# Optimization experiments

Hardware: AMD Instinct MI355X
Metric: run time of the kernel (lower is better)

The kernel has to match this reference:

```python
import jax, jax.numpy as jnp
import numpy as np
from jax import lax

N, T, IN = 64, 1024, 64
H = 512
H2 = H // 2   # 256
H4 = H // 4   # 128
H10 = H // 10 # 51


def _lstm(x, Wih, Whh, bih, bhh):
    """PyTorch-style LSTM, batch_first. x: [N,T,in]. Returns hs [N,T,h], h_T, c_T."""
    n, t, _ = x.shape
    h = Whh.shape[1]
    b = bih + bhh

    def step(carry, xt):
        hprev, cprev = carry
        gates = xt @ Wih.T + hprev @ Whh.T + b
        i, f, g, o = jnp.split(gates, 4, axis=-1)
        i = jax.nn.sigmoid(i)
        f = jax.nn.sigmoid(f)
        g = jnp.tanh(g)
        o = jax.nn.sigmoid(o)
        c = f * cprev + i * g
        hnew = o * jnp.tanh(c)
        return (hnew, c), hnew

    h0 = jnp.zeros((n, h), x.dtype)
    c0 = jnp.zeros((n, h), x.dtype)
    (hT, cT), hs = lax.scan(step, (h0, c0), x.transpose(1, 0, 2))
    return hs.transpose(1, 0, 2), hT, cT


def _causal_self_attention(hs):
    """Unscaled dot-product causal attention, equivalent to the python loop."""
    n, t, h = hs.shape
    scores = jnp.einsum('nth,nsh->nts', hs, hs)  # [N,T,T]
    mask = jnp.tril(jnp.ones((t, t), bool))
    scores = jnp.where(mask[None], scores, -jnp.inf)
    attn = jax.nn.softmax(scores, axis=-1)
    return jnp.einsum('nts,nsh->nth', attn, hs)


def setup_inputs() -> dict:
    key = jax.random.key(0)
    ks = jax.random.split(key, 16)
    s = 0.05
    return {
        'x': jax.random.normal(ks[0], (N, T, IN), jnp.float32),
        'W_ih1': jax.random.normal(ks[1], (4 * H, IN), jnp.float32) * s,
        'W_hh1': jax.random.normal(ks[2], (4 * H, H), jnp.float32) * s,
        'b_ih1': jax.random.normal(ks[3], (4 * H,), jnp.float32) * s,
        'b_hh1': jax.random.normal(ks[4], (4 * H,), jnp.float32) * s,
        'W_ih2': jax.random.normal(ks[5], (4 * H2, H), jnp.float32) * s,
        'W_hh2': jax.random.normal(ks[6], (4 * H2, H2), jnp.float32) * s,
        'b_ih2': jax.random.normal(ks[7], (4 * H2,), jnp.float32) * s,
        'b_hh2': jax.random.normal(ks[8], (4 * H2,), jnp.float32) * s,
        'fc1_w': jax.random.normal(ks[9], (H4, 2 * H2), jnp.float32) * s,
        'fc1_b': jax.random.normal(ks[10], (H4,), jnp.float32) * s,
        'fc2_w': jax.random.normal(ks[11], (H10, H4), jnp.float32) * s,
        'fc2_b': jax.random.normal(ks[12], (H10,), jnp.float32) * s,
        'fc3_w': jax.random.normal(ks[13], (1, H10), jnp.float32) * s,
        'fc3_b': jax.random.normal(ks[14], (1,), jnp.float32) * s,
    }


def reference(x, W_ih1, W_hh1, b_ih1, b_hh1, W_ih2, W_hh2, b_ih2, b_hh2,
              fc1_w, fc1_b, fc2_w, fc2_b, fc3_w, fc3_b):
    out, h1, c1 = _lstm(x, W_ih1, W_hh1, b_ih1, b_hh1)     # [N,T,H]
    out, h2, c2 = _lstm(out, W_ih2, W_hh2, b_ih2, b_hh2)   # [N,T,H2]
    contexts = _causal_self_attention(out)                  # [N,T,H2]
    out = jnp.concatenate((contexts, out), axis=2)          # [N,T,2*H2]
    out = jax.nn.relu(out @ fc1_w.T + fc1_b)                # dropout_ratio=0 -> identity
    out = jax.nn.relu(out @ fc2_w.T + fc2_b)
    out = out @ fc3_w.T + fc3_b                              # [N,T,1]
    return out, h1, c1, h2, c2
```

## Files before the change

### kernel.cpp

```cpp
#include <hip/hip_runtime.h>
#include <hip/hip_bf16.h>

#define N_   64
#define T_   1024
#define IN_  64
#define H1_  512
#define H2_  256
#define NG   4
#define NU1  16
#define NU2  8
#define RING 8
#define RING2 4
#define SENT 0xAAAAAAAAu

typedef __bf16 bf16x8 __attribute__((ext_vector_type(8)));
typedef float  f32x4  __attribute__((ext_vector_type(4)));
typedef unsigned int u32x4 __attribute__((ext_vector_type(4)));
typedef unsigned short u16x8 __attribute__((ext_vector_type(8)));
typedef unsigned long long u64;
typedef __hip_bfloat16 bf16_t;

#define OFF_FLG2  8192u
#define OFF_QUE   12288u
#define ZERO_BYTES 16384u
#define OFF_H1R   16384u
#define OFF_H2R   540672u
#define OFF_XB    671744u
#define OFF_W1    9060352u
#define OFF_W2    11419648u
#define OFF_B1    12992512u
#define OFF_B2    13000704u
#define OFF_FC1W  13004800u
#define OFF_FC2W  13135872u
#define OFF_HS2   13152256u
#define OFF_BURN  46706688u

__device__ __forceinline__ bf16x8 ld16(const bf16_t* p) {
  u32x4 u = *reinterpret_cast<const u32x4*>(p);
  return __builtin_bit_cast(bf16x8, u);
}
__device__ __forceinline__ u64 ld64_mall(const void* p) {
  return __hip_atomic_load((const u64*)p, __ATOMIC_RELAXED, __HIP_MEMORY_SCOPE_AGENT);
}
__device__ __forceinline__ void st4_mall(bf16_t* p, unsigned v) {
  __hip_atomic_store((unsigned*)p, v, __ATOMIC_RELAXED, __HIP_MEMORY_SCOPE_AGENT);
}
__device__ __forceinline__ unsigned ldflag(unsigned* p) {
  return __hip_atomic_load(p, __ATOMIC_RELAXED, __HIP_MEMORY_SCOPE_AGENT);
}
__device__ __forceinline__ bool sentok(u64 w) {
  return ((unsigned)w != SENT) && ((unsigned)(w >> 32) != SENT);
}
__device__ __forceinline__ f32x4 mfma_bf16(bf16x8 a, bf16x8 b, f32x4 c) {
  return __builtin_amdgcn_mfma_f32_16x16x32_bf16(a, b, c, 0, 0, 0);
}
__device__ __forceinline__ float sigf(float x) { return 1.f / (1.f + __expf(-x)); }
__device__ __forceinline__ float tanh_fast(float x) {
  float e = __expf(-2.f * fabsf(x));
  float r = (1.f - e) / (1.f + e);
  return x < 0.f ? -r : r;
}
__device__ __forceinline__ unsigned short bf16_bits(float v) {
  __hip_bfloat16 b = __float2bfloat16(v);
  return *reinterpret_cast<unsigned short*>(&b);
}

__global__ void setup_kernel(const float* __restrict__ x,
    const float* __restrict__ Wih1, const float* __restrict__ Whh1,
    const float* __restrict__ bih1, const float* __restrict__ bhh1,
    const float* __restrict__ Wih2, const float* __restrict__ Whh2,
    const float* __restrict__ bih2, const float* __restrict__ bhh2,
    const float* __restrict__ fc1w, const float* __restrict__ fc2w,
    char* __restrict__ ws)
{
  bf16_t* xb = (bf16_t*)(ws + OFF_XB);
  bf16_t* w1 = (bf16_t*)(ws + OFF_W1);
  bf16_t* w2 = (bf16_t*)(ws + OFF_W2);
  float*  b1 = (float*)(ws + OFF_B1);
  float*  b2 = (float*)(ws + OFF_B2);
  bf16_t* f1 = (bf16_t*)(ws + OFF_FC1W);
  bf16_t* f2 = (bf16_t*)(ws + OFF_FC2W);
  const long E0 = 4194304, E1 = E0 + 1179648, E2 = E1 + 786432,
             E3 = E2 + 2048, E4 = E3 + 1024, E5 = E4 + 65536, E6 = E5 + 8192;
  for (long i = blockIdx.x * (long)blockDim.x + threadIdx.x; i < E6;
       i += (long)gridDim.x * blockDim.x) {
    if (i < E0) {
      xb[i] = __float2bfloat16(x[i]);
    } else if (i < E1) {
      long idx = i - E0; long j = idx / 576, k = idx % 576;
      float v = (k < 64) ? Wih1[j * 64 + k] : Whh1[j * 512 + (k - 64)];
      w1[idx] = __float2bfloat16(v);
    } else if (i < E2) {
      long idx = i - E1; long j = idx / 768, k = idx % 768;
      float v = (k < 512) ? Wih2[j * 512 + k] : Whh2[j * 256 + (k - 512)];
      w2[idx] = __float2bfloat16(v);
    } else if (i < E3) {
      long idx = i - E2; b1[idx] = bih1[idx] + bhh1[idx];
    } else if (i < E4) {
      long idx = i - E3; b2[idx] = bih2[idx] + bhh2[idx];
    } else if (i < E5) {
      long idx = i - E4; f1[idx] = __float2bfloat16(fc1w[idx]);
    } else {
      long idx = i - E5; long j = idx / 128, k = idx % 128;
      f2[idx] = __float2bfloat16(j < 51 ? fc2w[j * 128 + k] : 0.f);
    }
  }
}

__global__ __launch_bounds__(256, 1) void fused_kernel(char* __restrict__ ws,
    const float* __restrict__ fc1b, const float* __restrict__ fc2b,
    const float* __restrict__ fc3w, const float* __restrict__ fc3b,
    float* __restrict__ dout)
{
  const bf16_t* xb  = (const bf16_t*)(ws + OFF_XB);
  const bf16_t* W1  = (const bf16_t*)(ws + OFF_W1);
  const bf16_t* W2  = (const bf16_t*)(ws + OFF_W2);
  const float*  b1  = (const float*)(ws + OFF_B1);
  const float*  b2  = (const float*)(ws + OFF_B2);
  bf16_t* h1r = (bf16_t*)(ws + OFF_H1R);
  bf16_t* h2r = (bf16_t*)(ws + OFF_H2R);
  bf16_t* hs2 = (bf16_t*)(ws + OFF_HS2);
  unsigned* flag2 = (unsigned*)(ws + OFF_FLG2);

  __shared__ __align__(16) char smem[55296];

  const int tid  = threadIdx.x;
  const int wave = tid >> 6;
  const int lane = tid & 63;
  const int l15  = lane & 15;
  const int quad = lane >> 4;
  const int bx   = blockIdx.x;
  const f32x4 z = {0.f, 0.f, 0.f, 0.f};

  if (bx < NG * NU1) {
    const int g = bx >> 4, u = bx & 15, u0 = u * 32;
    bf16_t* hstage = (bf16_t*)smem;
    float*  gbuf   = (float*)(smem + 18688);
    bf16x8 wf[18][2];
    #pragma unroll
    for (int i = 0; i < 18; ++i)
      #pragma unroll
      for (int nt = 0; nt < 2; ++nt)
        wf[i][nt] = ld16(W1 + (size_t)(wave * H1_ + u0 + nt * 16 + l15) * 576 + i * 32 + quad * 8);

    const int sr = tid >> 4;
    const int myp = tid & 15;
    const int row = tid >> 4, ui = (tid & 15) * 2;
    const int nrow = g * 16 + row;
    unsigned* bp = flag2 + (g * NU2 + (tid & 7)) * 32;
    float bi[2], bff[2], bg[2], bo[2], creg[2];
    #pragma unroll
    for (int j = 0; j < 2; ++j) {
      int ug = u0 + ui + j;
      bi[j]  = b1[ug];         bff[j] = b1[H1_ + ug];
      bg[j]  = b1[2*H1_ + ug]; bo[j]  = b1[3*H1_ + ug];
      creg[j] = 0.f;
    }
    #pragma unroll
    for (int s = 0; s < RING; ++s)
      st4_mall(h1r + ((size_t)(g * RING + s) * 16 + row) * 512 + u0 + ui, SENT);

    #pragma unroll 1
    for (int t = 0; t < T_; ++t) {
      {
        u64 xv = *(const u64*)(xb + ((size_t)(g*16 + sr) * T_ + t) * IN_ + myp * 4);
        *(u64*)(hstage + sr * 584 + myp * 4) = xv;
      }
      if (t >= 7)
        while ((int)ldflag(bp) < t - 6) __builtin_amdgcn_s_sleep(1);
      if (t == 0) {
        #pragma unroll
        for (int k = 0; k < 8; ++k)
          *(u64*)(hstage + sr * 584 + 64 + myp * 32 + k * 4) = 0ull;
      } else {
        const u64* src = (const u64*)(h1r + ((size_t)(g * RING + ((t-1) & 7)) * 16 + sr) * 512 + myp * 32);
        u64 w[8];
        for (;;) {
          #pragma unroll
          for (int k = 0; k < 8; ++k) w[k] = ld64_mall(src + k);
          bool ok = true;
          #pragma unroll
          for (int k = 0; k < 8; ++k) ok &= sentok(w[k]);
          if (ok) break;
        }
        #pragma unroll
        for (int k = 0; k < 8; ++k)
          *(u64*)(hstage + sr * 584 + 64 + myp * 32 + k * 4) = w[k];
      }
      __syncthreads();
      st4_mall(h1r + ((size_t)(g * RING + ((t+1) & 7)) * 16 + row) * 512 + u0 + ui, SENT);
      f32x4 acc[2] = {z, z}, acd[2] = {z, z};
      #pragma unroll
      for (int ki = 0; ki < 9; ++ki) {
        bf16x8 aw = ld16(hstage + l15 * 584 + ki * 32 + quad * 8);
        acc[0] = mfma_bf16(aw, wf[ki][0], acc[0]);
        acc[1] = mfma_bf16(aw, wf[ki][1], acc[1]);
      }
      #pragma unroll
      for (int ki = 9; ki < 18; ++ki) {
        bf16x8 aw = ld16(hstage + l15 * 584 + ki * 32 + quad * 8);
        acd[0] = mfma_bf16(aw, wf[ki][0], acd[0]);
        acd[1] = mfma_bf16(aw, wf[ki][1], acd[1]);
      }
      acc[0] += acd[0]; acc[1] += acd[1];
      #pragma unroll
      for (int nt = 0; nt < 2; ++nt)
        #pragma unroll
        for (int r = 0; r < 4; ++r)
          gbuf[(wave * 16 + quad * 4 + r) * 33 + nt * 16 + l15] = acc[nt][r];
      __syncthreads();
      {
        unsigned pack = 0;
        float hv[2];
        #pragma unroll
        for (int j = 0; j < 2; ++j) {
          int col = ui + j;
          float iv = sigf(gbuf[(0*16 + row) * 33 + col] + bi[j]);
          float fv = sigf(gbuf[(1*16 + row) * 33 + col] + bff[j]);
          float gv = tanh_fast(gbuf[(2*16 + row) * 33 + col] + bg[j]);
          float ov = sigf(gbuf[(3*16 + row) * 33 + col] + bo[j]);
          float c = fv * creg[j] + iv * gv;
          creg[j] = c;
          float h = ov * tanh_fast(c);
          hv[j] = h;
          pack |= (unsigned)bf16_bits(h) << (16 * j);
        }
        st4_mall(h1r + ((size_t)(g * RING + (t & 7)) * 16 + row) * 512 + u0 + ui, pack);
        if (t == T_ - 1) {
          #pragma unroll
          for (int j = 0; j < 2; ++j) {
            dout[65536 + nrow * H1_ + u0 + ui + j] = hv[j];
            dout[98304 + nrow * H1_ + u0 + ui + j] = creg[j];
          }
        }
      }
    }
  } else if (bx < NG * NU1 + NG * NU2) {
    const int b2x = bx - NG * NU1;
    const int g = b2x >> 3, u = b2x & 7, u0 = u * 32;
    bf16_t* hstage = (bf16_t*)smem;
    float*  gbuf   = (float*)(smem + 25088);
    bf16x8 wf[24][2];
    #pragma unroll
    for (int i = 0; i < 24; ++i)
      #pragma unroll
      for (int nt = 0; nt < 2; ++nt)
        wf[i][nt] = ld16(W2 + (size_t)(wave * H2_ + u0 + nt * 16 + l15) * 768 + i * 32 + quad * 8);

    const int sr = tid >> 4;
    const int q  = tid & 15;
    const int row = tid >> 4, ui = (tid & 15) * 2;
    const int nrow = g * 16 + row;
    unsigned* myflag = flag2 + (g * NU2 + u) * 32;
    float bi[2], bff[2], bg[2], bo[2], creg[2];
    #pragma unroll
    for (int j = 0; j < 2; ++j) {
      int ug = u0 + ui + j;
      bi[j]  = b2[ug];         bff[j] = b2[H2_ + ug];
      bg[j]  = b2[2*H2_ + ug]; bo[j]  = b2[3*H2_ + ug];
      creg[j] = 0.f;
    }
    #pragma unroll
    for (int s = 0; s < RING2; ++s)
      st4_mall(h2r + ((size_t)(g * RING2 + s) * 16 + row) * 256 + u0 + ui, SENT);

    u64 pf[8];
    #pragma unroll 1
    for (int t = 0; t < T_; ++t) {
      {
        const u64* s1 = (const u64*)(h1r + ((size_t)(g * RING + (t & 7)) * 16 + sr) * 512 + q * 32);
        bool good = (t > 0);
        if (good) {
          #pragma unroll
          for (int k = 0; k < 8; ++k) good &= sentok(pf[k]);
        }
        if (!good) {
          for (;;) {
            #pragma unroll
            for (int k = 0; k < 8; ++k) pf[k] = ld64_mall(s1 + k);
            bool ok = true;
            #pragma unroll
            for (int k = 0; k < 8; ++k) ok &= sentok(pf[k]);
            if (ok) break;
          }
        }
        #pragma unroll
        for (int k = 0; k < 8; ++k)
          *(u64*)(hstage + sr * 784 + q * 32 + k * 4) = pf[k];
      }
      if (t == 0) {
        #pragma unroll
        for (int k = 0; k < 4; ++k)
          *(u64*)(hstage + sr * 784 + 512 + q * 16 + k * 4) = 0ull;
      } else {
        const u64* s2 = (const u64*)(h2r + ((size_t)(g * RING2 + ((t-1) & 3)) * 16 + sr) * 256 + q * 16);
        u64 w[4];
        for (;;) {
          #pragma unroll
          for (int k = 0; k < 4; ++k) w[k] = ld64_mall(s2 + k);
          bool ok = true;
          #pragma unroll
          for (int k = 0; k < 4; ++k) ok &= sentok(w[k]);
          if (ok) break;
        }
        #pragma unroll
        for (int k = 0; k < 4; ++k)
          *(u64*)(hstage + sr * 784 + 512 + q * 16 + k * 4) = w[k];
      }
      __syncthreads();
      if (tid == 0 && t > 0)
        __hip_atomic_store(myflag, (unsigned)t, __ATOMIC_RELAXED, __HIP_MEMORY_SCOPE_AGENT);
      st4_mall(h2r + ((size_t)(g * RING2 + ((t+1) & 3)) * 16 + row) * 256 + u0 + ui, SENT);
      f32x4 acc[2] = {z, z}, acd[2] = {z, z};
      #pragma unroll
      for (int ki = 0; ki < 12; ++ki) {
        bf16x8 aw = ld16(hstage + l15 * 784 + ki * 32 + quad * 8);
        acc[0] = mfma_bf16(aw, wf[ki][0], acc[0]);
        acc[1] = mfma_bf16(aw, wf[ki][1], acc[1]);
      }
      #pragma unroll
      for (int ki = 12; ki < 24; ++ki) {
        bf16x8 aw = ld16(hstage + l15 * 784 + ki * 32 + quad * 8);
        acd[0] = mfma_bf16(aw, wf[ki][0], acd[0]);
        acd[1] = mfma_bf16(aw, wf[ki][1], acd[1]);
      }
      acc[0] += acd[0]; acc[1] += acd[1];
      #pragma unroll
      for (int nt = 0; nt < 2; ++nt)
        #pragma unroll
        for (int r = 0; r < 4; ++r)
          gbuf[(wave * 16 + quad * 4 + r) * 33 + nt * 16 + l15] = acc[nt][r];
      __syncthreads();
      {
        unsigned pack = 0;
        float hv[2];
        #pragma unroll
        for (int j = 0; j < 2; ++j) {
          int col = ui + j;
          float iv = sigf(gbuf[(0*16 + row) * 33 + col] + bi[j]);
          float fv = sigf(gbuf[(1*16 + row) * 33 + col] + bff[j]);
          float gv = tanh_fast(gbuf[(2*16 + row) * 33 + col] + bg[j]);
          float ov = sigf(gbuf[(3*16 + row) * 33 + col] + bo[j]);
          float c = fv * creg[j] + iv * gv;
          creg[j] = c;
          float h = ov * tanh_fast(c);
          hv[j] = h;
          pack |= (unsigned)bf16_bits(h) << (16 * j);
        }
        st4_mall(h2r + ((size_t)(g * RING2 + (t & 3)) * 16 + row) * 256 + u0 + ui, pack);
        st4_mall(hs2 + ((size_t)nrow * T_ + t) * H2_ + u0 + ui, pack);
        if (t == T_ - 1) {
          #pragma unroll
          for (int j = 0; j < 2; ++j) {
            dout[131072 + nrow * H2_ + u0 + ui + j] = hv[j];
            dout[147456 + nrow * H2_ + u0 + ui + j] = creg[j];
          }
        }
      }
      if (t + 1 < T_) {
        const u64* nx = (const u64*)(h1r + ((size_t)(g * RING + ((t+1) & 7)) * 16 + sr) * 512 + q * 32);
        #pragma unroll
        for (int k = 0; k < 8; ++k) pf[k] = ld64_mall(nx + k);
      }
    }
    __syncthreads();
    if (tid == 0)
      __hip_atomic_store(myflag, (unsigned)T_, __ATOMIC_RELAXED, __HIP_MEMORY_SCOPE_AGENT);
  }

  __syncthreads();
  {
    const bf16_t* f1w = (const bf16_t*)(ws + OFF_FC1W);
    const bf16_t* f2w = (const bf16_t*)(ws + OFF_FC2W);
    unsigned* queue = (unsigned*)(ws + OFF_QUE);
    unsigned short* vtile = (unsigned short*)smem;
    bf16_t* plds   = (bf16_t*)(smem + 36864);
    bf16_t* ctxlds = (bf16_t*)smem;
    bf16_t* act1   = (bf16_t*)(smem + 36864);
    float*  act2   = (float*)smem;
    volatile int* itemslot = (volatile int*)(smem + 55040);
    float burn = 1.0f;

    for (;;) {
      if (tid == 0) *itemslot = (int)atomicAdd(queue, 1u);
      __syncthreads();
      const int item = *itemslot;
      __syncthreads();
      if (item >= 1024) break;
      const int qt = item >> 6, n = item & 63, q0 = qt * 64, gg = n >> 4;

      {
        const int need = q0 + 64;
        if (tid < 64) {
          unsigned* p = (lane < NU2) ? flag2 + (gg * NU2 + lane) * 32 : nullptr;
          bool ok = (p == nullptr) || ((int)ldflag(p) >= need);
          while (!__all(ok)) {
            #pragma unroll
            for (int k = 0; k < 32; ++k) burn = fmaf(burn, 1.0000001f, 1e-7f);
            ok = (p == nullptr) || ((int)ldflag(p) >= need);
          }
        }
        __syncthreads();
      }

      bf16x8 aq[8];
      #pragma unroll
      for (int ks = 0; ks < 8; ++ks)
        aq[ks] = ld16(hs2 + ((size_t)n * T_ + q0 + wave * 16 + l15) * H2_ + ks * 32 + quad * 8);
      f32x4 o[16];
      #pragma unroll
      for (int ct = 0; ct < 16; ++ct) o[ct] = z;
      float m_run[4], l_run[4];
      #pragma unroll
      for (int r = 0; r < 4; ++r) { m_run[r] = -1e30f; l_run[r] = 0.f; }
      bf16_t* pw = plds + wave * 1152;

      #pragma unroll 1
      for (int st = 0; st <= qt; ++st) {
        const int s0 = st * 64;
        __syncthreads();
        #pragma unroll
        for (int it = 0; it < 8; ++it) {
          int s  = (tid >> 3) + (it & 1) * 32;
          int c0 = (tid & 7) * 8 + (it >> 1) * 64;
          u16x8 v = *reinterpret_cast<const u16x8*>(
              (const unsigned short*)hs2 + ((size_t)n * T_ + s0 + s) * H2_ + c0);
          #pragma unroll
          for (int j = 0; j < 8; ++j) {
            int ch = c0 + j;
            int sw = (s & 7) | ((((s >> 3) ^ (ch >> 3)) & 7) << 3);
            vtile[ch * 72 + sw] = v[j];
          }
        }
        __syncthreads();
        f32x4 sc[4] = {z, z, z, z};
        #pragma unroll
        for (int ks = 0; ks < 8; ++ks) {
          #pragma unroll
          for (int nt = 0; nt < 4; ++nt) {
            bf16x8 bk = ld16(hs2 + ((size_t)n * T_ + s0 + nt * 16 + l15) * H2_ + ks * 32 + quad * 8);
            sc[nt] = mfma_bf16(aq[ks], bk, sc[nt]);
          }
        }
        if (st == qt) {
          int qg = q0 + wave * 16 + quad * 4;
          #pragma unroll
          for (int nt = 0; nt < 4; ++nt) {
            int sg = s0 + nt * 16 + l15;
            #pragma unroll
            for (int r = 0; r < 4; ++r)
              if (sg > qg + r) sc[nt][r] = -1e30f;
          }
        }
        float alpha[4];
        #pragma unroll
        for (int r = 0; r < 4; ++r) {
          float tm = fmaxf(fmaxf(sc[0][r], sc[1][r]), fmaxf(sc[2][r], sc[3][r]));
          tm = fmaxf(tm, __shfl_xor(tm, 1, 16));
          tm = fmaxf(tm, __shfl_xor(tm, 2, 16));
          tm = fmaxf(tm, __shfl_xor(tm, 4, 16));
          tm = fmaxf(tm, __shfl_xor(tm, 8, 16));
          float mnew = fmaxf(m_run[r], tm);
          alpha[r] = __expf(m_run[r] - mnew);
          m_run[r] = mnew;
          float ts = 0.f;
          #pragma unroll
          for (int nt = 0; nt < 4; ++nt) {
            float p = __expf(sc[nt][r] - mnew);
            sc[nt][r] = p;
            ts += p;
          }
          ts += __shfl_xor(ts, 1, 16);
          ts += __shfl_xor(ts, 2, 16);
          ts += __shfl_xor(ts, 4, 16);
          ts += __shfl_xor(ts, 8, 16);
          l_run[r] = l_run[r] * alpha[r] + ts;
        }
        #pragma unroll
        for (int ct = 0; ct < 16; ++ct)
          #pragma unroll
          for (int r = 0; r < 4; ++r)
            o[ct][r] *= alpha[r];
        #pragma unroll
        for (int nt = 0; nt < 4; ++nt)
          #pragma unroll
          for (int r = 0; r < 4; ++r)
            pw[(quad * 4 + r) * 72 + nt * 16 + l15] = __float2bfloat16(sc[nt][r]);
        #pragma unroll
        for (int ks2 = 0; ks2 < 2; ++ks2) {
          bf16x8 ap = ld16(pw + l15 * 72 + ks2 * 32 + quad * 8);
          #pragma unroll
          for (int ct = 0; ct < 16; ++ct) {
            int ch = ct * 16 + l15;
            int blk = ((ks2 * 4 + quad) ^ (ch >> 3)) & 7;
            bf16x8 bv = ld16((bf16_t*)vtile + ch * 72 + blk * 8);
            o[ct] = mfma_bf16(ap, bv, o[ct]);
          }
        }
      }
      __syncthreads();
      float inv[4];
      #pragma unroll
      for (int r = 0; r < 4; ++r) inv[r] = 1.f / l_run[r];
      #pragma unroll
      for (int ct = 0; ct < 16; ++ct)
        #pragma unroll
        for (int r = 0; r < 4; ++r)
          ctxlds[(wave * 16 + quad * 4 + r) * 264 + ct * 16 + l15] =
              __float2bfloat16(o[ct][r] * inv[r]);
      __syncthreads();

      f32x4 a1[4][2];
      #pragma unroll
      for (int mt = 0; mt < 4; ++mt) { a1[mt][0] = z; a1[mt][1] = z; }
      #pragma unroll
      for (int ks = 0; ks < 16; ++ks) {
        bf16x8 af[4];
        if (ks < 8) {
          #pragma unroll
          for (int mt = 0; mt < 4; ++mt)
            af[mt] = ld16(ctxlds + (mt * 16 + l15) * 264 + ks * 32 + quad * 8);
        } else {
          #pragma unroll
          for (int mt = 0; mt < 4; ++mt)
            af[mt] = ld16(hs2 + ((size_t)n * T_ + q0 + mt * 16 + l15) * H2_ + (ks - 8) * 32 + quad * 8);
        }
        #pragma unroll
        for (int nt = 0; nt < 2; ++nt) {
          bf16x8 bw = ld16(f1w + (size_t)(wave * 32 + nt * 16 + l15) * 512 + ks * 32 + quad * 8);
          #pragma unroll
          for (int mt = 0; mt < 4; ++mt)
            a1[mt][nt] = mfma_bf16(af[mt], bw, a1[mt][nt]);
        }
      }
      #pragma unroll
      for (int mt = 0; mt < 4; ++mt)
        #pragma unroll
        for (int nt = 0; nt < 2; ++nt)
          #pragma unroll
          for (int r = 0; r < 4; ++r) {
            int ch = wave * 32 + nt * 16 + l15;
            float v = a1[mt][nt][r] + fc1b[ch];
            act1[(mt * 16 + quad * 4 + r) * 136 + ch] = __float2bfloat16(fmaxf(v, 0.f));
          }
      __syncthreads();

      f32x4 a2[4] = {z, z, z, z};
      #pragma unroll
      for (int ks = 0; ks < 4; ++ks) {
        bf16x8 bw = ld16(f2w + (wave * 16 + l15) * 128 + ks * 32 + quad * 8);
        #pragma unroll
        for (int mt = 0; mt < 4; ++mt) {
          bf16x8 af = ld16(act1 + (mt * 16 + l15) * 136 + ks * 32 + quad * 8);
          a2[mt] = mfma_bf16(af, bw, a2[mt]);
        }
      }
      __syncthreads();
      #pragma unroll
      for (int mt = 0; mt < 4; ++mt)
        #pragma unroll
        for (int r = 0; r < 4; ++r) {
          int ch = wave * 16 + l15;
          int rw = mt * 16 + quad * 4 + r;
          float v = a2[mt][r] + (ch < 51 ? fc2b[ch] : 0.f);
          act2[rw * 68 + ch] = fmaxf(v, 0.f);
        }
      __syncthreads();
      if (tid < 64) {
        float s = fc3b[0];
        for (int c = 0; c < 51; ++c) s += act2[tid * 68 + c] * fc3w[c];
        dout[(size_t)n * T_ + q0 + tid] = s;
      }
      __syncthreads();
    }
    if (burn == 0.1234567f)
      ((float*)(ws + OFF_BURN))[tid] = burn;
  }
}

extern "C" void kernel_launch(void* const* d_in, const int* in_sizes, int n_in,
                              void* d_out, int out_size, void* d_ws, size_t ws_size,
                              hipStream_t stream) {
  (void)in_sizes; (void)n_in; (void)out_size; (void)ws_size;
  const float* x    = (const float*)d_in[0];
  const float* Wih1 = (const float*)d_in[1];
  const float* Whh1 = (const float*)d_in[2];
  const float* bih1 = (const float*)d_in[3];
  const float* bhh1 = (const float*)d_in[4];
  const float* Wih2 = (const float*)d_in[5];
  const float* Whh2 = (const float*)d_in[6];
  const float* bih2 = (const float*)d_in[7];
  const float* bhh2 = (const float*)d_in[8];
  const float* fc1w = (const float*)d_in[9];
  const float* fc1b = (const float*)d_in[10];
  const float* fc2w = (const float*)d_in[11];
  const float* fc2b = (const float*)d_in[12];
  const float* fc3w = (const float*)d_in[13];
  const float* fc3b = (const float*)d_in[14];
  char* ws  = (char*)d_ws;
  float* out = (float*)d_out;

  hipMemsetAsync(ws, 0, ZERO_BYTES, stream);
  setup_kernel<<<2048, 256, 0, stream>>>(x, Wih1, Whh1, bih1, bhh1,
                                         Wih2, Whh2, bih2, bhh2, fc1w, fc2w, ws);
  fused_kernel<<<256, 256, 0, stream>>>(ws, fc1b, fc2b, fc3w, fc3b, out);
}
```

Measured before the change: 3.095 ms.

## Interleave gate weights so LSTM cell math runs in registers, drop gbuf sync

```diff
diff --git a/kernel.cpp b/kernel.cpp
--- a/kernel.cpp
+++ b/kernel.cpp
@@ -87,11 +87,15 @@
     if (i < E0) {
       xb[i] = __float2bfloat16(x[i]);
     } else if (i < E1) {
-      long idx = i - E0; long j = idx / 576, k = idx % 576;
+      long idx = i - E0; long jj = idx / 576, k = idx % 576;
+      long u = jj >> 7, w = (jj >> 5) & 3, c = jj & 31;
+      long j = (c >> 3) * 512 + u * 32 + w * 8 + (c & 7);
       float v = (k < 64) ? Wih1[j * 64 + k] : Whh1[j * 512 + (k - 64)];
       w1[idx] = __float2bfloat16(v);
     } else if (i < E2) {
-      long idx = i - E1; long j = idx / 768, k = idx % 768;
+      long idx = i - E1; long jj = idx / 768, k = idx % 768;
+      long u = jj >> 7, w = (jj >> 5) & 3, c = jj & 31;
+      long j = (c >> 3) * 256 + u * 32 + w * 8 + (c & 7);
       float v = (k < 512) ? Wih2[j * 512 + k] : Whh2[j * 256 + (k - 512)];
       w2[idx] = __float2bfloat16(v);
     } else if (i < E3) {
@@ -134,44 +138,40 @@
 
   if (bx < NG * NU1) {
     const int g = bx >> 4, u = bx & 15, u0 = u * 32;
-    bf16_t* hstage = (bf16_t*)smem;
-    float*  gbuf   = (float*)(smem + 18688);
+    bf16_t* hst0 = (bf16_t*)smem;
+    bf16_t* hst1 = (bf16_t*)(smem + 18688);
     bf16x8 wf[18][2];
     #pragma unroll
     for (int i = 0; i < 18; ++i)
       #pragma unroll
       for (int nt = 0; nt < 2; ++nt)
-        wf[i][nt] = ld16(W1 + (size_t)(wave * H1_ + u0 + nt * 16 + l15) * 576 + i * 32 + quad * 8);
+        wf[i][nt] = ld16(W1 + (size_t)((u * 4 + wave) * 32 + nt * 16 + l15) * 576 + i * 32 + quad * 8);
 
     const int sr = tid >> 4;
     const int myp = tid & 15;
     const int row = tid >> 4, ui = (tid & 15) * 2;
-    const int nrow = g * 16 + row;
     unsigned* bp = flag2 + (g * NU2 + (tid & 7)) * 32;
-    float bi[2], bff[2], bg[2], bo[2], creg[2];
-    #pragma unroll
-    for (int j = 0; j < 2; ++j) {
-      int ug = u0 + ui + j;
-      bi[j]  = b1[ug];         bff[j] = b1[H1_ + ug];
-      bg[j]  = b1[2*H1_ + ug]; bo[j]  = b1[3*H1_ + ug];
-      creg[j] = 0.f;
-    }
+    const int ul = l15 & 7;
+    const int myU = u0 + wave * 8 + ul;
+    const bool hi = (l15 >> 3) != 0;
+    const int row0 = quad * 4 + (hi ? 2 : 0);
+    const int nrow0 = g * 16 + row0;
+    const float bi  = b1[myU],        bf_ = b1[512 + myU];
+    const float bg_ = b1[1024 + myU], bo_ = b1[1536 + myU];
+    float creg0 = 0.f, creg1 = 0.f;
     #pragma unroll
     for (int s = 0; s < RING; ++s)
       st4_mall(h1r + ((size_t)(g * RING + s) * 16 + row) * 512 + u0 + ui, SENT);
 
     #pragma unroll 1
     for (int t = 0; t < T_; ++t) {
-      {
-        u64 xv = *(const u64*)(xb + ((size_t)(g*16 + sr) * T_ + t) * IN_ + myp * 4);
-        *(u64*)(hstage + sr * 584 + myp * 4) = xv;
-      }
-      if (t >= 7)
-        while ((int)ldflag(bp) < t - 6) __builtin_amdgcn_s_sleep(1);
+      bf16_t* hst = (t & 1) ? hst1 : hst0;
+      u64 xv = *(const u64*)(xb + ((size_t)(g*16 + sr) * T_ + t) * IN_ + myp * 4);
+      unsigned fvreg = ldflag(bp);
       if (t == 0) {
         #pragma unroll
         for (int k = 0; k < 8; ++k)
-          *(u64*)(hstage + sr * 584 + 64 + myp * 32 + k * 4) = 0ull;
+          *(u64*)(hst + sr * 584 + 64 + myp * 32 + k * 4) = 0ull;
       } else {
         const u64* src = (const u64*)(h1r + ((size_t)(g * RING + ((t-1) & 7)) * 16 + sr) * 512 + myp * 32);
         u64 w[8];
@@ -185,81 +185,85 @@
         }
         #pragma unroll
         for (int k = 0; k < 8; ++k)
-          *(u64*)(hstage + sr * 584 + 64 + myp * 32 + k * 4) = w[k];
-      }
-      __syncthreads();
-      st4_mall(h1r + ((size_t)(g * RING + ((t+1) & 7)) * 16 + row) * 512 + u0 + ui, SENT);
+          *(u64*)(hst + sr * 584 + 64 + myp * 32 + k * 4) = w[k];
+      }
+      *(u64*)(hst + sr * 584 + myp * 4) = xv;
+      if (t >= 6 && (int)fvreg < t - 5) {
+        while ((int)ldflag(bp) < t - 5) __builtin_amdgcn_s_sleep(1);
+      }
+      __syncthreads();
+      st4_mall(h1r + ((size_t)(g * RING + ((t+2) & 7)) * 16 + row) * 512 + u0 + ui, SENT);
       f32x4 acc[2] = {z, z}, acd[2] = {z, z};
       #pragma unroll
       for (int ki = 0; ki < 9; ++ki) {
-        bf16x8 aw = ld16(hstage + l15 * 584 + ki * 32 + quad * 8);
+        bf16x8 aw = ld16(hst + l15 * 584 + ki * 32 + quad * 8);
         acc[0] = mfma_bf16(aw, wf[ki][0], acc[0]);
         acc[1] = mfma_bf16(aw, wf[ki][1], acc[1]);
       }
       #pragma unroll
       for (int ki = 9; ki < 18; ++ki) {
-        bf16x8 aw = ld16(hstage + l15 * 584 + ki * 32 + quad * 8);
+        bf16x8 aw = ld16(hst + l15 * 584 + ki * 32 + quad * 8);
         acd[0] = mfma_bf16(aw, wf[ki][0], acd[0]);
         acd[1] = mfma_bf16(aw, wf[ki][1], acd[1]);
       }
       acc[0] += acd[0]; acc[1] += acd[1];
-      #pragma unroll
-      for (int nt = 0; nt < 2; ++nt)
-        #pragma unroll
-        for (int r = 0; r < 4; ++r)
-          gbuf[(wave * 16 + quad * 4 + r) * 33 + nt * 16 + l15] = acc[nt][r];
-      __syncthreads();
-      {
-        unsigned pack = 0;
-        float hv[2];
-        #pragma unroll
-        for (int j = 0; j < 2; ++j) {
-          int col = ui + j;
-          float iv = sigf(gbuf[(0*16 + row) * 33 + col] + bi[j]);
-          float fv = sigf(gbuf[(1*16 + row) * 33 + col] + bff[j]);
-          float gv = tanh_fast(gbuf[(2*16 + row) * 33 + col] + bg[j]);
-          float ov = sigf(gbuf[(3*16 + row) * 33 + col] + bo[j]);
-          float c = fv * creg[j] + iv * gv;
-          creg[j] = c;
-          float h = ov * tanh_fast(c);
-          hv[j] = h;
-          pack |= (unsigned)bf16_bits(h) << (16 * j);
-        }
-        st4_mall(h1r + ((size_t)(g * RING + (t & 7)) * 16 + row) * 512 + u0 + ui, pack);
-        if (t == T_ - 1) {
-          #pragma unroll
-          for (int j = 0; j < 2; ++j) {
-            dout[65536 + nrow * H1_ + u0 + ui + j] = hv[j];
-            dout[98304 + nrow * H1_ + u0 + ui + j] = creg[j];
-          }
-        }
+      float a0r[4], a1r[4], x0r[4], x1r[4];
+      #pragma unroll
+      for (int r = 0; r < 4; ++r) {
+        a0r[r] = acc[0][r]; a1r[r] = acc[1][r];
+        x0r[r] = __shfl_xor(a0r[r], 8, 16);
+        x1r[r] = __shfl_xor(a1r[r], 8, 16);
+      }
+      float gi0 = hi ? x0r[2] : a0r[0], gf0 = hi ? a0r[2] : x0r[0];
+      float gg0 = hi ? x1r[2] : a1r[0], go0 = hi ? a1r[2] : x1r[0];
+      float gi1 = hi ? x0r[3] : a0r[1], gf1 = hi ? a0r[3] : x0r[1];
+      float gg1 = hi ? x1r[3] : a1r[1], go1 = hi ? a1r[3] : x1r[1];
+      float c0 = sigf(gf0 + bf_) * creg0 + sigf(gi0 + bi) * tanh_fast(gg0 + bg_);
+      creg0 = c0;
+      float h0 = sigf(go0 + bo_) * tanh_fast(c0);
+      float c1 = sigf(gf1 + bf_) * creg1 + sigf(gi1 + bi) * tanh_fast(gg1 + bg_);
+      creg1 = c1;
+      float h1v = sigf(go1 + bo_) * tanh_fast(c1);
+      float n0 = __shfl_xor(h0, 1, 16);
+      float n1 = __shfl_xor(h1v, 1, 16);
+      if ((l15 & 1) == 0) {
+        bf16_t* base = h1r + (size_t)(g * RING + (t & 7)) * 16 * 512;
+        st4_mall(base + row0 * 512 + myU,
+                 (unsigned)bf16_bits(h0) | ((unsigned)bf16_bits(n0) << 16));
+        st4_mall(base + (row0 + 1) * 512 + myU,
+                 (unsigned)bf16_bits(h1v) | ((unsigned)bf16_bits(n1) << 16));
+      }
+      if (t == T_ - 1) {
+        dout[65536 + nrow0 * H1_ + myU]       = h0;
+        dout[65536 + (nrow0 + 1) * H1_ + myU] = h1v;
+        dout[98304 + nrow0 * H1_ + myU]       = creg0;
+        dout[98304 + (nrow0 + 1) * H1_ + myU] = creg1;
       }
     }
   } else if (bx < NG * NU1 + NG * NU2) {
     const int b2x = bx - NG * NU1;
     const int g = b2x >> 3, u = b2x & 7, u0 = u * 32;
-    bf16_t* hstage = (bf16_t*)smem;
-    float*  gbuf   = (float*)(smem + 25088);
+    bf16_t* hst0 = (bf16_t*)smem;
+    bf16_t* hst1 = (bf16_t*)(smem + 25088);
     bf16x8 wf[24][2];
     #pragma unroll
     for (int i = 0; i < 24; ++i)
       #pragma unroll
       for (int nt = 0; nt < 2; ++nt)
-        wf[i][nt] = ld16(W2 + (size_t)(wave * H2_ + u0 + nt * 16 + l15) * 768 + i * 32 + quad * 8);
+        wf[i][nt] = ld16(W2 + (size_t)((u * 4 + wave) * 32 + nt * 16 + l15) * 768 + i * 32 + quad * 8);
 
     const int sr = tid >> 4;
     const int q  = tid & 15;
     const int row = tid >> 4, ui = (tid & 15) * 2;
-    const int nrow = g * 16 + row;
     unsigned* myflag = flag2 + (g * NU2 + u) * 32;
-    float bi[2], bff[2], bg[2], bo[2], creg[2];
-    #pragma unroll
-    for (int j = 0; j < 2; ++j) {
-      int ug = u0 + ui + j;
-      bi[j]  = b2[ug];         bff[j] = b2[H2_ + ug];
-      bg[j]  = b2[2*H2_ + ug]; bo[j]  = b2[3*H2_ + ug];
-      creg[j] = 0.f;
-    }
+    const int ul = l15 & 7;
+    const int myU = u0 + wave * 8 + ul;
+    const bool hi = (l15 >> 3) != 0;
+    const int row0 = quad * 4 + (hi ? 2 : 0);
+    const int nrow0 = g * 16 + row0;
+    const float bi  = b2[myU],       bf_ = b2[256 + myU];
+    const float bg_ = b2[512 + myU], bo_ = b2[768 + myU];
+    float creg0 = 0.f, creg1 = 0.f;
     #pragma unroll
     for (int s = 0; s < RING2; ++s)
       st4_mall(h2r + ((size_t)(g * RING2 + s) * 16 + row) * 256 + u0 + ui, SENT);
@@ -267,6 +271,7 @@
     u64 pf[8];
     #pragma unroll 1
     for (int t = 0; t < T_; ++t) {
+      bf16_t* hst = (t & 1) ? hst1 : hst0;
       {
         const u64* s1 = (const u64*)(h1r + ((size_t)(g * RING + (t & 7)) * 16 + sr) * 512 + q * 32);
         bool good = (t > 0);
@@ -286,12 +291,12 @@
         }
         #pragma unroll
         for (int k = 0; k < 8; ++k)
-          *(u64*)(hstage + sr * 784 + q * 32 + k * 4) = pf[k];
+          *(u64*)(hst + sr * 784 + q * 32 + k * 4) = pf[k];
       }
       if (t == 0) {
         #pragma unroll
         for (int k = 0; k < 4; ++k)
-          *(u64*)(hstage + sr * 784 + 512 + q * 16 + k * 4) = 0ull;
+          *(u64*)(hst + sr * 784 + 512 + q * 16 + k * 4) = 0ull;
       } else {
         const u64* s2 = (const u64*)(h2r + ((size_t)(g * RING2 + ((t-1) & 3)) * 16 + sr) * 256 + q * 16);
         u64 w[4];
@@ -305,57 +310,59 @@
         }
         #pragma unroll
         for (int k = 0; k < 4; ++k)
-          *(u64*)(hstage + sr * 784 + 512 + q * 16 + k * 4) = w[k];
+          *(u64*)(hst + sr * 784 + 512 + q * 16 + k * 4) = w[k];
       }
       __syncthreads();
       if (tid == 0 && t > 0)
         __hip_atomic_store(myflag, (unsigned)t, __ATOMIC_RELAXED, __HIP_MEMORY_SCOPE_AGENT);
-      st4_mall(h2r + ((size_t)(g * RING2 + ((t+1) & 3)) * 16 + row) * 256 + u0 + ui, SENT);
+      st4_mall(h2r + ((size_t)(g * RING2 + ((t+2) & 3)) * 16 + row) * 256 + u0 + ui, SENT);
       f32x4 acc[2] = {z, z}, acd[2] = {z, z};
       #pragma unroll
       for (int ki = 0; ki < 12; ++ki) {
-        bf16x8 aw = ld16(hstage + l15 * 784 + ki * 32 + quad * 8);
+        bf16x8 aw = ld16(hst + l15 * 784 + ki * 32 + quad * 8);
         acc[0] = mfma_bf16(aw, wf[ki][0], acc[0]);
         acc[1] = mfma_bf16(aw, wf[ki][1], acc[1]);
       }
       #pragma unroll
       for (int ki = 12; ki < 24; ++ki) {
-        bf16x8 aw = ld16(hstage + l15 * 784 + ki * 32 + quad * 8);
+        bf16x8 aw = ld16(hst + l15 * 784 + ki * 32 + quad * 8);
         acd[0] = mfma_bf16(aw, wf[ki][0], acd[0]);
         acd[1] = mfma_bf16(aw, wf[ki][1], acd[1]);
       }
       acc[0] += acd[0]; acc[1] += acd[1];
-      #pragma unroll
-      for (int nt = 0; nt < 2; ++nt)
-        #pragma unroll
-        for (int r = 0; r < 4; ++r)
-          gbuf[(wave * 16 + quad * 4 + r) * 33 + nt * 16 + l15] = acc[nt][r];
-      __syncthreads();
-      {
-        unsigned pack = 0;
-        float hv[2];
-        #pragma unroll
-        for (int j = 0; j < 2; ++j) {
-          int col = ui + j;
-          float iv = sigf(gbuf[(0*16 + row) * 33 + col] + bi[j]);
-          float fv = sigf(gbuf[(1*16 + row) * 33 + col] + bff[j]);
-          float gv = tanh_fast(gbuf[(2*16 + row) * 33 + col] + bg[j]);
-          float ov = sigf(gbuf[(3*16 + row) * 33 + col] + bo[j]);
-          float c = fv * creg[j] + iv * gv;
-          creg[j] = c;
-          float h = ov * tanh_fast(c);
-          hv[j] = h;
-          pack |= (unsigned)bf16_bits(h) << (16 * j);
-        }
-        st4_mall(h2r + ((size_t)(g * RING2 + (t & 3)) * 16 + row) * 256 + u0 + ui, pack);
-        st4_mall(hs2 + ((size_t)nrow * T_ + t) * H2_ + u0 + ui, pack);
-        if (t == T_ - 1) {
-          #pragma unroll
-          for (int j = 0; j < 2; ++j) {
-            dout[131072 + nrow * H2_ + u0 + ui + j] = hv[j];
-            dout[147456 + nrow * H2_ + u0 + ui + j] = creg[j];
-          }
-        }
+      float a0r[4], a1r[4], x0r[4], x1r[4];
+      #pragma unroll
+      for (int r = 0; r < 4; ++r) {
+        a0r[r] = acc[0][r]; a1r[r] = acc[1][r];
+        x0r[r] = __shfl_xor(a0r[r], 8, 16);
+        x1r[r] = __shfl_xor(a1r[r], 8, 16);
+      }
+      float gi0 = hi ? x0r[2] : a0r[0], gf0 = hi ? a0r[2] : x0r[0];
+      float gg0 = hi ? x1r[2] : a1r[0], go0 = hi ? a1r[2] : x1r[0];
+      float gi1 = hi ? x0r[3] : a0r[1], gf1 = hi ? a0r[3] : x0r[1];
+      float gg1 = hi ? x1r[3] : a1r[1], go1 = hi ? a1r[3] : x1r[1];
+      float c0 = sigf(gf0 + bf_) * creg0 + sigf(gi0 + bi) * tanh_fast(gg0 + bg_);
+      creg0 = c0;
+      float h0 = sigf(go0 + bo_) * tanh_fast(c0);
+      float c1 = sigf(gf1 + bf_) * creg1 + sigf(gi1 + bi) * tanh_fast(gg1 + bg_);
+      creg1 = c1;
+      float h1v = sigf(go1 + bo_) * tanh_fast(c1);
+      float n0 = __shfl_xor(h0, 1, 16);
+      float n1 = __shfl_xor(h1v, 1, 16);
+      if ((l15 & 1) == 0) {
+        unsigned p0 = (unsigned)bf16_bits(h0) | ((unsigned)bf16_bits(n0) << 16);
+        unsigned p1 = (unsigned)bf16_bits(h1v) | ((unsigned)bf16_bits(n1) << 16);
+        bf16_t* b2r = h2r + (size_t)(g * RING2 + (t & 3)) * 16 * 256;
+        st4_mall(b2r + row0 * 256 + myU, p0);
+        st4_mall(b2r + (row0 + 1) * 256 + myU, p1);
+        st4_mall(hs2 + ((size_t)nrow0 * T_ + t) * H2_ + myU, p0);
+        st4_mall(hs2 + ((size_t)(nrow0 + 1) * T_ + t) * H2_ + myU, p1);
+      }
+      if (t == T_ - 1) {
+        dout[131072 + nrow0 * H2_ + myU]       = h0;
+        dout[131072 + (nrow0 + 1) * H2_ + myU] = h1v;
+        dout[147456 + nrow0 * H2_ + myU]       = creg0;
+        dout[147456 + (nrow0 + 1) * H2_ + myU] = creg1;
       }
       if (t + 1 < T_) {
         const u64* nx = (const u64*)(h1r + ((size_t)(g * RING + ((t+1) & 7)) * 16 + sr) * 512 + q * 32);
```

Measured after the change: 3.169 ms. 1.02x slower.
